# Optimization experiments

Hardware: AMD Instinct MI355X
Metric: run time of the kernel (lower is better)

## Reference

```python
import jax, jax.numpy as jnp
import numpy as np

B, T = 512, 8192
MIN_SPEECH = 1.0      # config.min_speech_frames
MAX_EXPAND = 3.0      # config.max_speech_expand
TOPK_RATIO = 0.35     # config.pause_topk_ratio
MIN_BW = 0.1          # config.pause_min_boundary_weight
BIAS_W = 0.15         # config.pause_boundary_bias_weight
TEMP = 0.12           # config.pause_soft_temperature


def setup_inputs() -> dict:
    key = jax.random.key(0)
    ks = jax.random.split(key, 9)
    return {
        "dur_anchor_src": jax.random.uniform(ks[0], (B, T)) * 10.0,
        "dur_logratio_unit": jax.random.normal(ks[1], (B, T)) * 0.3,
        "pause_weight_unit": jax.random.uniform(ks[2], (B, T)),
        "boundary_latent": jax.random.uniform(ks[3], (B, T)),
        "unit_mask": jnp.ones((B, T), jnp.float32),
        "speech_budget_win": jax.random.uniform(ks[4], (B,)) * (2.0 * T),
        "pause_budget_win": jax.random.uniform(ks[5], (B,)) * (0.2 * T),
        "previous_speech_exec": jax.random.uniform(ks[6], (B, T)) * 3.0,
        "previous_pause_exec": jax.random.uniform(ks[7], (B, T)),
        "commit_frontier": jax.random.randint(ks[8], (B,), 0, T // 2),
    }


def reference(dur_anchor_src, dur_logratio_unit, pause_weight_unit, boundary_latent,
              unit_mask, speech_budget_win, pause_budget_win,
              previous_speech_exec, previous_pause_exec, commit_frontier):
    Tn = unit_mask.shape[1]
    pos = jnp.arange(Tn)[None, :]                                  # [1,T]
    prefix_mask = (pos < commit_frontier[:, None]).astype(unit_mask.dtype)  # [B,T]
    tail_mask = unit_mask * (1.0 - prefix_mask)

    # ---- lift budgets to feasible region (reuse_prefix=True) ----
    prefix_speech = jnp.sum(previous_speech_exec * unit_mask * prefix_mask, axis=1)
    prefix_pause = jnp.sum(previous_pause_exec * unit_mask * prefix_mask, axis=1)
    min_tail_speech = jnp.sum(tail_mask, axis=1) * MIN_SPEECH
    speech_budget = jnp.maximum(speech_budget_win, prefix_speech + min_tail_speech)
    pause_budget = jnp.maximum(pause_budget_win, prefix_pause)

    # ---- project speech ----
    anchor = jnp.maximum(dur_anchor_src, MIN_SPEECH)
    base = anchor * jnp.exp(dur_logratio_unit)
    candidate = jnp.clip(base, MIN_SPEECH, anchor * MAX_EXPAND) * unit_mask
    speech_prefix = previous_speech_exec * unit_mask * prefix_mask
    rem_s = speech_budget - jnp.sum(speech_prefix, axis=1)          # [B]
    cand_tail_sum = jnp.maximum(jnp.sum(candidate * tail_mask, axis=1), 1e-6)
    do_s = (jnp.sum(tail_mask, axis=1) > 0) & (rem_s > 0)
    scale_s = jnp.where(do_s, rem_s / cand_tail_sum, 0.0)[:, None]
    speech = (speech_prefix + candidate * scale_s * tail_mask) * unit_mask

    # ---- project pause (soft top-k selection) ----
    scores = (jnp.maximum(pause_weight_unit, 0.0)
              + BIAS_W * (MIN_BW + jnp.maximum(boundary_latent, 0.0))) * unit_mask
    keep_k = max(1, int(round(Tn * TOPK_RATIO)))                    # static, < T
    topv = jax.lax.top_k(scores, keep_k)[0]                         # [B,keep_k]
    thr = jax.lax.stop_gradient(topv[:, -1])[:, None]               # detached threshold
    gate = jax.nn.sigmoid((scores - thr) / TEMP)
    sparse = scores * gate * unit_mask

    pause_prefix = previous_pause_exec * unit_mask * prefix_mask
    rem_p = jnp.maximum(pause_budget - jnp.sum(pause_prefix, axis=1), 0.0)
    tail_sum = jnp.sum(tail_mask, axis=1)
    fallback = tail_mask / jnp.maximum(tail_sum, 1.0)[:, None]
    tail_cand = jnp.maximum(sparse, 0.0) * tail_mask + fallback * 1e-6
    denom = jnp.maximum(jnp.sum(tail_cand * tail_mask, axis=1), 1e-6)
    do_p = (tail_sum > 0) & (rem_p > 0)
    scale_p = jnp.where(do_p, rem_p / denom, 0.0)[:, None]
    pause = (pause_prefix + tail_cand * scale_p * tail_mask) * unit_mask

    return jnp.stack([speech, pause])                               # [2,B,T]
```

## Files before the change

### kernel.cpp

```cpp
#include <hip/hip_runtime.h>

#define T_DIM 8192
#define NTH 512
#define NWAVE 8
#define GROUPS 4
#define NBIN 2048
#define KEEP_K 2867
#define KSCALE 32768.0f
#define INV_KSCALE (1.0f / 32768.0f)
#define BINW (32.0f / 32768.0f)

typedef float nt4 __attribute__((ext_vector_type(4)));

__global__ __launch_bounds__(NTH, 2) void srp_kernel(
    const float* __restrict__ g_anchor,
    const float* __restrict__ g_lr,
    const float* __restrict__ g_pw,
    const float* __restrict__ g_bl,
    const float* __restrict__ g_mask,
    const float* __restrict__ g_sbud,
    const float* __restrict__ g_pbud,
    const float* __restrict__ g_psp,
    const float* __restrict__ g_ppa,
    const int*  __restrict__ g_front,
    float* __restrict__ g_out,
    int n_rows)
{
    constexpr float MIN_SPEECH = 1.0f;
    constexpr float MAX_EXPAND = 3.0f;
    constexpr float MIN_BW = 0.1f;
    constexpr float BIAS_W = 0.15f;
    constexpr float INV_TEMP = 1.0f / 0.12f;

    __shared__ unsigned s_cnt[NBIN];
    __shared__ float    s_ws[NBIN];
    __shared__ float wred[NWAVE][5];
    __shared__ float s_scal[6];
    __shared__ float sh_thr;

    const int b = blockIdx.x;
    const int tid = threadIdx.x;
    const int wave = tid >> 6;
    const int lane = tid & 63;
    const long long row = (long long)b * T_DIM;
    const int f = g_front[b];
    const float sbud = g_sbud[b];
    const float pbud = g_pbud[b];

    #pragma unroll
    for (int i = 0; i < NBIN / NTH; ++i) {
        s_cnt[tid + NTH * i] = 0u;
        s_ws[tid + NTH * i]  = 0.f;
    }
    __syncthreads();

    float SC1[16];
    float PM[16];
    unsigned kp[8];
    float a_ps = 0.f, a_pp = 0.f, a_ts = 0.f, a_cs = 0.f, a_t2 = 0.f;

    #pragma unroll
    for (int g = 0; g < GROUPS; ++g) {
        const int t0 = g * 2048 + (tid << 2);
        const float4 an4 = *reinterpret_cast<const float4*>(g_anchor + row + t0);
        const float4 lr4 = *reinterpret_cast<const float4*>(g_lr + row + t0);
        const float4 pw4 = *reinterpret_cast<const float4*>(g_pw + row + t0);
        const float4 bl4 = *reinterpret_cast<const float4*>(g_bl + row + t0);
        const float4 mk4 = *reinterpret_cast<const float4*>(g_mask + row + t0);
        const float4 ps4 = *reinterpret_cast<const float4*>(g_psp + row + t0);
        const float4 pp4 = *reinterpret_cast<const float4*>(g_ppa + row + t0);
        unsigned kk0 = 0u, kk1 = 0u;
        #pragma unroll
        for (int c = 0; c < 4; ++c) {
            const int i = (g << 2) + c;
            const int t = t0 + c;
            const float m   = (&mk4.x)[c];
            const float pre = (t < f) ? 1.0f : 0.0f;
            const float tl  = m * (1.0f - pre);
            const float ps = (&ps4.x)[c];
            const float pp = (&pp4.x)[c];
            a_ps += ps * m * pre;
            a_pp += pp * m * pre;
            a_ts += tl;
            a_t2 += tl * tl;
            const float an = fmaxf((&an4.x)[c], MIN_SPEECH);
            const float cand = fminf(fmaxf(an * __expf((&lr4.x)[c]), MIN_SPEECH),
                                     an * MAX_EXPAND) * m;
            a_cs += cand * tl;
            const float s = (fmaxf((&pw4.x)[c], 0.0f)
                             + BIAS_W * (MIN_BW + fmaxf((&bl4.x)[c], 0.0f))) * m;
            const unsigned key = (unsigned)fminf(s * KSCALE, 65535.0f);
            atomicAdd(&s_cnt[key >> 5], 1u);
            const float w = s * m * tl * tl;
            if (w > 0.0f) atomicAdd(&s_ws[key >> 5], w);
            if (c < 2) kk0 |= key << (16 * c);
            else       kk1 |= key << (16 * (c - 2));
            SC1[i] = ps * m * m * pre + cand * tl * m;
            PM[i]  = (t < f) ? pp * m * m : m;
        }
        kp[2 * g]     = kk0;
        kp[2 * g + 1] = kk1;
    }

    #pragma unroll
    for (int o = 32; o > 0; o >>= 1) {
        a_ps += __shfl_down(a_ps, o, 64);
        a_pp += __shfl_down(a_pp, o, 64);
        a_ts += __shfl_down(a_ts, o, 64);
        a_cs += __shfl_down(a_cs, o, 64);
        a_t2 += __shfl_down(a_t2, o, 64);
    }
    if (lane == 0) {
        wred[wave][0] = a_ps; wred[wave][1] = a_pp;
        wred[wave][2] = a_ts; wred[wave][3] = a_cs;
        wred[wave][4] = a_t2;
    }
    __syncthreads();

    if (tid == 64) {
        float ps = 0.f, pp = 0.f, ts = 0.f, cs = 0.f, t2 = 0.f;
        for (int w = 0; w < NWAVE; ++w) {
            ps += wred[w][0]; pp += wred[w][1]; ts += wred[w][2];
            cs += wred[w][3]; t2 += wred[w][4];
        }
        const float sb = fmaxf(sbud, ps + ts * MIN_SPEECH);
        const float pb = fmaxf(pbud, pp);
        const float rem_s = sb - ps;
        const float cts = fmaxf(cs, 1e-6f);
        s_scal[0] = (ts > 0.0f && rem_s > 0.0f) ? (rem_s / cts) : 0.0f;
        s_scal[1] = fmaxf(pb - pp, 0.0f);
        s_scal[2] = ts;
        s_scal[3] = 1e-6f / fmaxf(ts, 1.0f);
        s_scal[5] = t2;
    }
    if (wave == 0) {
        const int base = NBIN - 32 * (lane + 1);
        unsigned csum = 0;
        #pragma unroll
        for (int i = 0; i < 32; ++i) csum += s_cnt[base + i];
        unsigned tot = csum;
        #pragma unroll
        for (int off = 1; off < 64; off <<= 1) {
            const unsigned n = __shfl_up(tot, off, 64);
            if (lane >= off) tot += n;
        }
        const unsigned excl = tot - csum;
        if (excl < KEEP_K && excl + csum >= KEEP_K) {
            const unsigned need = KEEP_K - excl;
            unsigned c = 0;
            int bin = base;
            for (int i = 31; i >= 0; --i) {
                c += s_cnt[base + i];
                if (c >= need) { bin = base + i; break; }
            }
            sh_thr = (float)bin * BINW;
        }
    }
    __syncthreads();

    const float thr = sh_thr;
    const float scale_s = s_scal[0];
    const float inv_ts6 = s_scal[3];

    #pragma unroll
    for (int g = 0; g < GROUPS; ++g) {
        const int t0 = g * 2048 + (tid << 2);
        nt4 vs;
        #pragma unroll
        for (int c = 0; c < 4; ++c) {
            const int i = (g << 2) + c;
            const int t = t0 + c;
            vs[c] = (t < f) ? SC1[i] : SC1[i] * scale_s;
        }
        __builtin_nontemporal_store(vs, reinterpret_cast<nt4*>(g_out + row + t0));
    }

    float a_d = 0.0f;
    #pragma unroll
    for (int i = 0; i < NBIN / NTH; ++i) {
        const int bin = tid + NTH * i;
        const float w = s_ws[bin];
        const float sc = ((float)bin + 0.5f) * BINW;
        a_d += w / (1.0f + __expf(-(sc - thr) * INV_TEMP));
    }
    #pragma unroll
    for (int o = 32; o > 0; o >>= 1) a_d += __shfl_down(a_d, o, 64);
    if (lane == 0) wred[wave][0] = a_d;
    __syncthreads();

    float dsum = s_scal[5] * inv_ts6;
    #pragma unroll
    for (int w = 0; w < NWAVE; ++w) dsum += wred[w][0];
    const float denom = fmaxf(dsum, 1e-6f);
    const float scale_p = (s_scal[2] > 0.0f && s_scal[1] > 0.0f)
                          ? (s_scal[1] / denom) : 0.0f;

    const long long out_off = (long long)n_rows * T_DIM;
    #pragma unroll
    for (int g = 0; g < GROUPS; ++g) {
        const int t0 = g * 2048 + (tid << 2);
        const unsigned kk0 = kp[2 * g], kk1 = kp[2 * g + 1];
        const unsigned kk[4] = { kk0 & 0xFFFFu, kk0 >> 16, kk1 & 0xFFFFu, kk1 >> 16 };
        nt4 vp;
        #pragma unroll
        for (int c = 0; c < 4; ++c) {
            const int i = (g << 2) + c;
            const int t = t0 + c;
            const float pm = PM[i];
            const float s = (float)kk[c] * INV_KSCALE;
            const float gate = 1.0f / (1.0f + __expf(-(s - thr) * INV_TEMP));
            const float tailv = scale_p * pm * pm * pm * (s * gate * pm + inv_ts6);
            vp[c] = (t < f) ? pm : tailv;
        }
        __builtin_nontemporal_store(vp, reinterpret_cast<nt4*>(g_out + out_off + row + t0));
    }
}

extern "C" void kernel_launch(void* const* d_in, const int* in_sizes, int n_in,
                              void* d_out, int out_size, void* d_ws, size_t ws_size,
                              hipStream_t stream) {
    const float* anchor = (const float*)d_in[0];
    const float* lr     = (const float*)d_in[1];
    const float* pw     = (const float*)d_in[2];
    const float* bl     = (const float*)d_in[3];
    const float* mask   = (const float*)d_in[4];
    const float* sbud   = (const float*)d_in[5];
    const float* pbud   = (const float*)d_in[6];
    const float* psp    = (const float*)d_in[7];
    const float* ppa    = (const float*)d_in[8];
    const int*   front  = (const int*)d_in[9];
    float* out = (float*)d_out;
    const int B = in_sizes[5];
    srp_kernel<<<B, NTH, 0, stream>>>(anchor, lr, pw, bl, mask, sbud, pbud,
                                      psp, ppa, front, out, B);
}
```

Before: 170.6 us.

## Move threshold and denominator work to wave 0, drop a barrier, raise occupancy

The input loads are now issued two groups at a time so more memory requests are in flight. Every thread now reduces the scalar partial sums itself instead of one thread publishing them through shared memory. Wave 0 finds the threshold, does the weighted-sigmoid denominator over all bins and computes the pause scale. Meanwhile the other waves write their speech outputs, which removes one block barrier and the reduction into wred. The launch-bounds occupancy hint rises from 2 to 4 blocks per CU, which may force register spills, and wave 0 now carries a serial 32-bin loop that could become the critical path.

Result: slower. 216.1 us (+26.6%).

```diff
diff --git a/kernel.cpp b/kernel.cpp
--- a/kernel.cpp
+++ b/kernel.cpp
@@ -3,7 +3,6 @@
 #define T_DIM 8192
 #define NTH 512
 #define NWAVE 8
-#define GROUPS 4
 #define NBIN 2048
 #define KEEP_K 2867
 #define KSCALE 32768.0f
@@ -12,7 +11,7 @@
 
 typedef float nt4 __attribute__((ext_vector_type(4)));
 
-__global__ __launch_bounds__(NTH, 2) void srp_kernel(
+__global__ __launch_bounds__(NTH, 4) void srp_kernel(
     const float* __restrict__ g_anchor,
     const float* __restrict__ g_lr,
     const float* __restrict__ g_pw,
@@ -35,8 +34,7 @@
     __shared__ unsigned s_cnt[NBIN];
     __shared__ float    s_ws[NBIN];
     __shared__ float wred[NWAVE][5];
-    __shared__ float s_scal[6];
-    __shared__ float sh_thr;
+    __shared__ float s_res[2];
 
     const int b = blockIdx.x;
     const int tid = threadIdx.x;
@@ -60,46 +58,55 @@
     float a_ps = 0.f, a_pp = 0.f, a_ts = 0.f, a_cs = 0.f, a_t2 = 0.f;
 
     #pragma unroll
-    for (int g = 0; g < GROUPS; ++g) {
-        const int t0 = g * 2048 + (tid << 2);
-        const float4 an4 = *reinterpret_cast<const float4*>(g_anchor + row + t0);
-        const float4 lr4 = *reinterpret_cast<const float4*>(g_lr + row + t0);
-        const float4 pw4 = *reinterpret_cast<const float4*>(g_pw + row + t0);
-        const float4 bl4 = *reinterpret_cast<const float4*>(g_bl + row + t0);
-        const float4 mk4 = *reinterpret_cast<const float4*>(g_mask + row + t0);
-        const float4 ps4 = *reinterpret_cast<const float4*>(g_psp + row + t0);
-        const float4 pp4 = *reinterpret_cast<const float4*>(g_ppa + row + t0);
-        unsigned kk0 = 0u, kk1 = 0u;
-        #pragma unroll
-        for (int c = 0; c < 4; ++c) {
-            const int i = (g << 2) + c;
-            const int t = t0 + c;
-            const float m   = (&mk4.x)[c];
-            const float pre = (t < f) ? 1.0f : 0.0f;
-            const float tl  = m * (1.0f - pre);
-            const float ps = (&ps4.x)[c];
-            const float pp = (&pp4.x)[c];
-            a_ps += ps * m * pre;
-            a_pp += pp * m * pre;
-            a_ts += tl;
-            a_t2 += tl * tl;
-            const float an = fmaxf((&an4.x)[c], MIN_SPEECH);
-            const float cand = fminf(fmaxf(an * __expf((&lr4.x)[c]), MIN_SPEECH),
-                                     an * MAX_EXPAND) * m;
-            a_cs += cand * tl;
-            const float s = (fmaxf((&pw4.x)[c], 0.0f)
-                             + BIAS_W * (MIN_BW + fmaxf((&bl4.x)[c], 0.0f))) * m;
-            const unsigned key = (unsigned)fminf(s * KSCALE, 65535.0f);
-            atomicAdd(&s_cnt[key >> 5], 1u);
-            const float w = s * m * tl * tl;
-            if (w > 0.0f) atomicAdd(&s_ws[key >> 5], w);
-            if (c < 2) kk0 |= key << (16 * c);
-            else       kk1 |= key << (16 * (c - 2));
-            SC1[i] = ps * m * m * pre + cand * tl * m;
-            PM[i]  = (t < f) ? pp * m * m : m;
-        }
-        kp[2 * g]     = kk0;
-        kp[2 * g + 1] = kk1;
+    for (int h = 0; h < 2; ++h) {
+        float4 an[2], lr[2], pw[2], bl[2], mk[2], ps[2], pp[2];
+        #pragma unroll
+        for (int g = 0; g < 2; ++g) {
+            const int t0 = (h * 2 + g) * 2048 + (tid << 2);
+            an[g] = *reinterpret_cast<const float4*>(g_anchor + row + t0);
+            lr[g] = *reinterpret_cast<const float4*>(g_lr + row + t0);
+            pw[g] = *reinterpret_cast<const float4*>(g_pw + row + t0);
+            bl[g] = *reinterpret_cast<const float4*>(g_bl + row + t0);
+            mk[g] = *reinterpret_cast<const float4*>(g_mask + row + t0);
+            ps[g] = *reinterpret_cast<const float4*>(g_psp + row + t0);
+            pp[g] = *reinterpret_cast<const float4*>(g_ppa + row + t0);
+        }
+        #pragma unroll
+        for (int g = 0; g < 2; ++g) {
+            const int t0 = (h * 2 + g) * 2048 + (tid << 2);
+            unsigned kk0 = 0u, kk1 = 0u;
+            #pragma unroll
+            for (int c = 0; c < 4; ++c) {
+                const int i = (h * 2 + g) * 4 + c;
+                const int t = t0 + c;
+                const float m   = (&mk[g].x)[c];
+                const float pre = (t < f) ? 1.0f : 0.0f;
+                const float tl  = m * (1.0f - pre);
+                const float psv = (&ps[g].x)[c];
+                const float ppv = (&pp[g].x)[c];
+                a_ps += psv * m * pre;
+                a_pp += ppv * m * pre;
+                a_ts += tl;
+                a_t2 += tl * tl;
+                const float anv = fmaxf((&an[g].x)[c], MIN_SPEECH);
+                const float cand = fminf(fmaxf(anv * __expf((&lr[g].x)[c]), MIN_SPEECH),
+                                         anv * MAX_EXPAND) * m;
+                a_cs += cand * tl;
+                const float s = (fmaxf((&pw[g].x)[c], 0.0f)
+                                 + BIAS_W * (MIN_BW + fmaxf((&bl[g].x)[c], 0.0f))) * m;
+                const unsigned key = (unsigned)fminf(s * KSCALE, 65535.0f);
+                atomicAdd(&s_cnt[key >> 5], 1u);
+                const float w = s * m * tl * tl;
+                if (w > 0.0f) atomicAdd(&s_ws[key >> 5], w);
+                if (c < 2) kk0 |= key << (16 * c);
+                else       kk1 |= key << (16 * (c - 2));
+                SC1[i] = psv * m * m * pre + cand * tl * m;
+                PM[i]  = (t < f) ? ppv * m * m : m;
+            }
+            kp[2 * (h * 2 + g) / 2 * 2 + 0] = kk0;
+            kp[(h * 2 + g) * 2]     = kk0;
+            kp[(h * 2 + g) * 2 + 1] = kk1;
+        }
     }
 
     #pragma unroll
@@ -117,22 +124,19 @@
     }
     __syncthreads();
 
-    if (tid == 64) {
-        float ps = 0.f, pp = 0.f, ts = 0.f, cs = 0.f, t2 = 0.f;
-        for (int w = 0; w < NWAVE; ++w) {
-            ps += wred[w][0]; pp += wred[w][1]; ts += wred[w][2];
-            cs += wred[w][3]; t2 += wred[w][4];
-        }
-        const float sb = fmaxf(sbud, ps + ts * MIN_SPEECH);
-        const float pb = fmaxf(pbud, pp);
-        const float rem_s = sb - ps;
-        const float cts = fmaxf(cs, 1e-6f);
-        s_scal[0] = (ts > 0.0f && rem_s > 0.0f) ? (rem_s / cts) : 0.0f;
-        s_scal[1] = fmaxf(pb - pp, 0.0f);
-        s_scal[2] = ts;
-        s_scal[3] = 1e-6f / fmaxf(ts, 1.0f);
-        s_scal[5] = t2;
-    }
+    float ps = 0.f, pp = 0.f, ts = 0.f, cs = 0.f, t2 = 0.f;
+    #pragma unroll
+    for (int w = 0; w < NWAVE; ++w) {
+        ps += wred[w][0]; pp += wred[w][1]; ts += wred[w][2];
+        cs += wred[w][3]; t2 += wred[w][4];
+    }
+    const float sb = fmaxf(sbud, ps + ts * MIN_SPEECH);
+    const float pb = fmaxf(pbud, pp);
+    const float rem_s = sb - ps;
+    const float scale_s = (ts > 0.0f && rem_s > 0.0f) ? (rem_s / fmaxf(cs, 1e-6f)) : 0.0f;
+    const float rem_p = fmaxf(pb - pp, 0.0f);
+    const float inv_ts6 = 1e-6f / fmaxf(ts, 1.0f);
+
     if (wave == 0) {
         const int base = NBIN - 32 * (lane + 1);
         unsigned csum = 0;
@@ -145,6 +149,7 @@
             if (lane >= off) tot += n;
         }
         const unsigned excl = tot - csum;
+        float thr_l = -1.0f;
         if (excl < KEEP_K && excl + csum >= KEEP_K) {
             const unsigned need = KEEP_K - excl;
             unsigned c = 0;
@@ -153,51 +158,62 @@
                 c += s_cnt[base + i];
                 if (c >= need) { bin = base + i; break; }
             }
-            sh_thr = (float)bin * BINW;
+            thr_l = (float)bin * BINW;
+        }
+        #pragma unroll
+        for (int off = 32; off > 0; off >>= 1)
+            thr_l = fmaxf(thr_l, __shfl_down(thr_l, off, 64));
+        thr_l = __shfl(thr_l, 0, 64);
+        float a_d = 0.0f;
+        #pragma unroll
+        for (int i = 0; i < 32; ++i) {
+            const int bin = lane + 64 * i;
+            const float w = s_ws[bin];
+            const float sc = ((float)bin + 0.5f) * BINW;
+            a_d += w / (1.0f + __expf(-(sc - thr_l) * INV_TEMP));
+        }
+        #pragma unroll
+        for (int off = 32; off > 0; off >>= 1) a_d += __shfl_down(a_d, off, 64);
+        if (lane == 0) {
+            const float denom = fmaxf(a_d + t2 * inv_ts6, 1e-6f);
+            s_res[0] = thr_l;
+            s_res[1] = (ts > 0.0f && rem_p > 0.0f) ? (rem_p / denom) : 0.0f;
+        }
+    } else {
+        #pragma unroll
+        for (int g = 0; g < 4; ++g) {
+            const int t0 = g * 2048 + (tid << 2);
+            nt4 vs;
+            #pragma unroll
+            for (int c = 0; c < 4; ++c) {
+                const int i = (g << 2) + c;
+                vs[c] = (t0 + c < f) ? SC1[i] : SC1[i] * scale_s;
+            }
+            __builtin_nontemporal_store(vs, reinterpret_cast<nt4*>(g_out + row + t0));
         }
     }
     __syncthreads();
 
-    const float thr = sh_thr;
-    const float scale_s = s_scal[0];
-    const float inv_ts6 = s_scal[3];
-
-    #pragma unroll
-    for (int g = 0; g < GROUPS; ++g) {
-        const int t0 = g * 2048 + (tid << 2);
-        nt4 vs;
-        #pragma unroll
-        for (int c = 0; c < 4; ++c) {
-            const int i = (g << 2) + c;
-            const int t = t0 + c;
-            vs[c] = (t < f) ? SC1[i] : SC1[i] * scale_s;
-        }
-        __builtin_nontemporal_store(vs, reinterpret_cast<nt4*>(g_out + row + t0));
-    }
-
-    float a_d = 0.0f;
-    #pragma unroll
-    for (int i = 0; i < NBIN / NTH; ++i) {
-        const int bin = tid + NTH * i;
-        const float w = s_ws[bin];
-        const float sc = ((float)bin + 0.5f) * BINW;
-        a_d += w / (1.0f + __expf(-(sc - thr) * INV_TEMP));
-    }
-    #pragma unroll
-    for (int o = 32; o > 0; o >>= 1) a_d += __shfl_down(a_d, o, 64);
-    if (lane == 0) wred[wave][0] = a_d;
-    __syncthreads();
-
-    float dsum = s_scal[5] * inv_ts6;
-    #pragma unroll
-    for (int w = 0; w < NWAVE; ++w) dsum += wred[w][0];
-    const float denom = fmaxf(dsum, 1e-6f);
-    const float scale_p = (s_scal[2] > 0.0f && s_scal[1] > 0.0f)
-                          ? (s_scal[1] / denom) : 0.0f;
-
+    const float thr = s_res[0];
+    const float scale_p = s_res[1];
     const long long out_off = (long long)n_rows * T_DIM;
-    #pragma unroll
-    for (int g = 0; g < GROUPS; ++g) {
+
+    if (wave == 0) {
+        #pragma unroll
+        for (int g = 0; g < 4; ++g) {
+            const int t0 = g * 2048 + (tid << 2);
+            nt4 vs;
+            #pragma unroll
+            for (int c = 0; c < 4; ++c) {
+                const int i = (g << 2) + c;
+                vs[c] = (t0 + c < f) ? SC1[i] : SC1[i] * scale_s;
+            }
+            __builtin_nontemporal_store(vs, reinterpret_cast<nt4*>(g_out + row + t0));
+        }
+    }
+
+    #pragma unroll
+    for (int g = 0; g < 4; ++g) {
         const int t0 = g * 2048 + (tid << 2);
         const unsigned kk0 = kp[2 * g], kk1 = kp[2 * g + 1];
         const unsigned kk[4] = { kk0 & 0xFFFFu, kk0 >> 16, kk1 & 0xFFFFu, kk1 >> 16 };
@@ -205,12 +221,11 @@
         #pragma unroll
         for (int c = 0; c < 4; ++c) {
             const int i = (g << 2) + c;
-            const int t = t0 + c;
             const float pm = PM[i];
             const float s = (float)kk[c] * INV_KSCALE;
             const float gate = 1.0f / (1.0f + __expf(-(s - thr) * INV_TEMP));
             const float tailv = scale_p * pm * pm * pm * (s * gate * pm + inv_ts6);
-            vp[c] = (t < f) ? pm : tailv;
+            vp[c] = (t0 + c < f) ? pm : tailv;
         }
         __builtin_nontemporal_store(vp, reinterpret_cast<nt4*>(g_out + out_off + row + t0));
     }
```
